# Kernel optimization log

Hardware: AMD Instinct MI355X
Metric: run time of the kernel (lower is better)

## Reference

```python
import jax, jax.numpy as jnp
import numpy as np

N_NODES = 50000
N_EDGES = 200000
D = 128
LN_EPS = 1e-5


def _layer_norm(x, g, b):
    mu = jnp.mean(x, axis=-1, keepdims=True)
    var = jnp.mean(jnp.square(x - mu), axis=-1, keepdims=True)
    return (x - mu) * jax.lax.rsqrt(var + LN_EPS) * g + b


def _mlp(x, W1, b1, W2, b2, W3, b3, g, beta):
    # 2 hidden ReLU layers + linear output + LayerNorm (MeshGraphNets style)
    h = jax.nn.relu(x @ W1 + b1)
    h = jax.nn.relu(h @ W2 + b2)
    h = h @ W3 + b3
    return _layer_norm(h, g, beta)


def setup_inputs() -> dict:
    key = jax.random.key(0)
    ks = jax.random.split(key, 12)
    d = {}
    d["node_features"] = jax.random.normal(ks[0], (N_NODES, D), dtype=jnp.float32)
    d["edge_features"] = jax.random.normal(ks[1], (N_EDGES, D), dtype=jnp.float32)
    d["senders"] = jax.random.randint(ks[2], (N_EDGES,), 0, N_NODES, dtype=jnp.int32)
    d["receivers"] = jax.random.randint(ks[3], (N_EDGES,), 0, N_NODES, dtype=jnp.int32)
    def lin(k, fan_in, fan_out):
        return jax.random.normal(k, (fan_in, fan_out), dtype=jnp.float32) / np.sqrt(fan_in)
    # edge MLP: [3D] -> D -> D -> D
    d["We1"] = lin(ks[4], 3 * D, D); d["be1"] = jnp.zeros((D,), jnp.float32)
    d["We2"] = lin(ks[5], D, D);     d["be2"] = jnp.zeros((D,), jnp.float32)
    d["We3"] = lin(ks[6], D, D);     d["be3"] = jnp.zeros((D,), jnp.float32)
    d["ge"] = jnp.ones((D,), jnp.float32); d["bege"] = jnp.zeros((D,), jnp.float32)
    # node MLP: [2D] -> D -> D -> D
    d["Wn1"] = lin(ks[7], 2 * D, D); d["bn1"] = jnp.zeros((D,), jnp.float32)
    d["Wn2"] = lin(ks[8], D, D);     d["bn2"] = jnp.zeros((D,), jnp.float32)
    d["Wn3"] = lin(ks[9], D, D);     d["bn3"] = jnp.zeros((D,), jnp.float32)
    d["gn"] = jnp.ones((D,), jnp.float32); d["begn"] = jnp.zeros((D,), jnp.float32)
    return d


def reference(node_features, edge_features, senders, receivers,
              We1, be1, We2, be2, We3, be3, ge, bege,
              Wn1, bn1, Wn2, bn2, Wn3, bn3, gn, begn):
    num_nodes = node_features.shape[0]
    # --- edge update: gather sender/receiver feats, concat, edge MLP ---
    edge_in = jnp.concatenate(
        [node_features[senders], node_features[receivers], edge_features], axis=-1)  # [E, 3D]
    new_edge = _mlp(edge_in, We1, be1, We2, be2, We3, be3, ge, bege)  # [E, D]
    # --- node update: scatter-sum aggregate, concat, node MLP ---
    agg = jax.ops.segment_sum(new_edge, receivers, num_segments=num_nodes)  # [N, D]
    node_in = jnp.concatenate([node_features, agg], axis=-1)  # [N, 2D]
    new_node = _mlp(node_in, Wn1, bn1, Wn2, bn2, Wn3, bn3, gn, begn)
    # --- residuals ---
    new_node = new_node + node_features
    new_edge = new_edge + edge_features
    return new_node, new_edge
```

## Files before the change

### kernel.cpp

```cpp
#include <hip/hip_runtime.h>
#include <hip/hip_bf16.h>

#define NNODES 50000
#define NEDGES 200000
#define DD 128
#define LN_EPS 1e-5f
#define NTH 256

typedef __attribute__((ext_vector_type(8))) short bf16x8;
typedef __attribute__((ext_vector_type(4))) float f32x4;
typedef __attribute__((ext_vector_type(16))) float f32x16;

template<int N> struct ic { static constexpr int value = N; };

__device__ __forceinline__ unsigned short bfr(float f) {
    union { __hip_bfloat16 b; unsigned short u; } v;
    v.b = __float2bfloat16(f);
    return v.u;
}

__global__ void build_wimg(const float* __restrict__ We1, const float* __restrict__ We2,
                           const float* __restrict__ We3, const float* __restrict__ Wn1,
                           const float* __restrict__ Wn2, const float* __restrict__ Wn3,
                           char* __restrict__ img_e, char* __restrict__ img_n) {
    int tid = blockIdx.x * NTH + threadIdx.x;
    const float* W; char* dst; int q;
    if      (tid <  6144) { W = We1; dst = img_e;             q = tid;         }
    else if (tid <  8192) { W = We2; dst = img_e + 12 * 8192; q = tid - 6144;  }
    else if (tid < 10240) { W = We3; dst = img_e + 16 * 8192; q = tid - 8192;  }
    else if (tid < 14336) { W = Wn1; dst = img_n;             q = tid - 10240; }
    else if (tid < 16384) { W = Wn2; dst = img_n + 8 * 8192;  q = tid - 14336; }
    else if (tid < 18432) { W = Wn3; dst = img_n + 12 * 8192; q = tid - 16384; }
    else return;
    int c = q >> 9, rem = q & 511;
    int nt = rem >> 7, r2 = rem & 127, ks = r2 >> 5, n32 = r2 & 31;
    int n = nt * 32 + n32;
    int k0 = c * 32 + ks * 8;
    unsigned short o[8];
    #pragma unroll
    for (int e = 0; e < 8; ++e)
        o[e] = bfr(W[(size_t)(k0 + e) * DD + n]);
    uint4 val;
    val.x = (unsigned)o[0] | ((unsigned)o[1] << 16);
    val.y = (unsigned)o[2] | ((unsigned)o[3] << 16);
    val.z = (unsigned)o[4] | ((unsigned)o[5] << 16);
    val.w = (unsigned)o[6] | ((unsigned)o[7] << 16);
    *(uint4*)(dst + (size_t)c * 8192 + nt * 2048 + ks * 512 + n32 * 16) = val;
}

__global__ void csr_histo(const int* __restrict__ recv, int* __restrict__ cnt) {
    int e = blockIdx.x * NTH + threadIdx.x;
    if (e < NEDGES) atomicAdd(&cnt[recv[e]], 1);
}

__global__ __launch_bounds__(1024)
void csr_scan(const int* __restrict__ cnt, int* __restrict__ off, int* __restrict__ cursor) {
    __shared__ int part[1024];
    const int t = threadIdx.x;
    const int CH = (NNODES + 1023) / 1024;
    const int base = t * CH;
    int s = 0;
    for (int i = 0; i < CH; ++i) {
        int idx = base + i;
        if (idx < NNODES) s += cnt[idx];
    }
    part[t] = s;
    __syncthreads();
    for (int d = 1; d < 1024; d <<= 1) {
        int v = (t >= d) ? part[t - d] : 0;
        __syncthreads();
        part[t] += v;
        __syncthreads();
    }
    int run = (t == 0) ? 0 : part[t - 1];
    for (int i = 0; i < CH; ++i) {
        int idx = base + i;
        if (idx < NNODES) {
            off[idx] = run; cursor[idx] = run;
            run += cnt[idx];
        }
    }
    if (t == 1023) off[NNODES] = NEDGES;
}

__global__ void csr_fill(const int* __restrict__ recv, int* __restrict__ cursor,
                         int* __restrict__ elist) {
    int e = blockIdx.x * NTH + threadIdx.x;
    if (e < NEDGES) {
        int p = atomicAdd(&cursor[recv[e]], 1);
        elist[p] = e;
    }
}

__global__ __launch_bounds__(NTH)
void aggregate(const unsigned* __restrict__ ybuf,
               const int* __restrict__ off, const int* __restrict__ elist,
               unsigned* __restrict__ aggb) {
    const int n = blockIdx.x * 4 + (threadIdx.x >> 6);
    const int l = threadIdx.x & 63;
    if (n >= NNODES) return;
    const int j0 = off[n], j1 = off[n + 1];
    float ax = 0.f, ay = 0.f, bx = 0.f, by = 0.f;
    int j = j0;
    for (; j + 1 < j1; j += 2) {
        unsigned v0 = ybuf[(size_t)elist[j] * 64 + l];
        unsigned v1 = ybuf[(size_t)elist[j + 1] * 64 + l];
        ax += __uint_as_float(v0 << 16);
        ay += __uint_as_float(v0 & 0xffff0000u);
        bx += __uint_as_float(v1 << 16);
        by += __uint_as_float(v1 & 0xffff0000u);
    }
    if (j < j1) {
        unsigned v = ybuf[(size_t)elist[j] * 64 + l];
        ax += __uint_as_float(v << 16);
        ay += __uint_as_float(v & 0xffff0000u);
    }
    float sx = ax + bx, sy = ay + by;
    aggb[(size_t)n * 64 + l] = (unsigned)bfr(sx) | ((unsigned)bfr(sy) << 16);
}

template<int MODE>
__global__ __launch_bounds__(NTH, 3)
void mgn_mfma(const float* __restrict__ nodef, const float* __restrict__ edgef,
              const int* __restrict__ senders, const int* __restrict__ receivers,
              const char* __restrict__ img,
              const float* __restrict__ b1, const float* __restrict__ b2,
              const float* __restrict__ b3,
              const float* __restrict__ gamma, const float* __restrict__ beta,
              const unsigned* __restrict__ aggb, unsigned* __restrict__ ybuf,
              float* __restrict__ outp)
{
    __shared__ char Hb[4 * 8192];

    const int t  = threadIdx.x;
    const int w  = t >> 6;
    const int l  = t & 63;
    const int ln = l & 31;
    const int hi = l >> 5;
    const int row0 = blockIdx.x * 128;
    const int gm = row0 + w * 32 + ln;
    constexpr int NROWS = (MODE == 0) ? NEDGES : NNODES;
    constexpr int NK1   = (MODE == 0) ? 12 : 8;
    constexpr int NCH   = NK1 + 8;
    const int gmc = gm < NROWS ? gm : NROWS - 1;
    const int sxH = ln & 15;

    int srow = 0, rrow = 0;
    if (MODE == 0) { srow = senders[gmc]; rrow = receivers[gmc]; }

    const f32x16 fz = {0.f,0.f,0.f,0.f,0.f,0.f,0.f,0.f,
                       0.f,0.f,0.f,0.f,0.f,0.f,0.f,0.f};
    f32x16 acc[4];
    #pragma unroll
    for (int nt = 0; nt < 4; ++nt) acc[nt] = fz;

    bf16x8 aslot[2][4];
    f32x4  bslot[2][4];

    auto loadA = [&](int h, bf16x8* dst) {
        const char* p = img + (size_t)(h >> 1) * 8192
                      + (size_t)(((h & 1) * 2 + hi) * 512) + ln * 16;
        #pragma unroll
        for (int nt = 0; nt < 4; ++nt)
            dst[nt] = *(const bf16x8*)(p + nt * 2048);
    };

    auto loadB = [&](auto CC, f32x4* dst) {
        constexpr int c = decltype(CC)::value;
        if constexpr (MODE == 1 && c >= 4) {
            const char* p = (const char*)aggb + (size_t)gmc * 256 + (c & 3) * 64 + hi * 16;
            dst[0] = *(const f32x4*)p;
            dst[2] = *(const f32x4*)(p + 32);
        } else {
            const float* base;
            if constexpr (MODE == 0) {
                base = (c < 4) ? nodef + (size_t)srow * DD
                     : (c < 8) ? nodef + (size_t)rrow * DD
                               : edgef + (size_t)gmc * DD;
            } else {
                base = nodef + (size_t)gmc * DD;
            }
            const float* p = base + (c & 3) * 32 + hi * 8;
            dst[0] = *(const f32x4*)p;
            dst[1] = *(const f32x4*)(p + 4);
            dst[2] = *(const f32x4*)(p + 16);
            dst[3] = *(const f32x4*)(p + 20);
        }
    };

    auto cvtB = [&](const f32x4* br) {
        bf16x8 r;
        #pragma unroll
        for (int i = 0; i < 4; ++i) r[i]     = (short)bfr(br[0][i]);
        #pragma unroll
        for (int i = 0; i < 4; ++i) r[4 + i] = (short)bfr(br[1][i]);
        return r;
    };

    auto loadBH = [&](int ks, int kh) {
        const char* p = Hb + w * 8192 + ln * 256
                      + (((ks * 4 + kh * 2 + hi) ^ sxH) << 4);
        return *(const bf16x8*)p;
    };

    auto getB = [&](auto CC, int kh) -> bf16x8 {
        constexpr int c = decltype(CC)::value;
        if constexpr (c >= NK1) {
            return loadBH((c - NK1) & 3, kh);
        } else if constexpr (MODE == 1 && c >= 4) {
            union { f32x4 f; bf16x8 h; } u;
            u.f = bslot[c & 1][kh * 2];
            return u.h;
        } else {
            return cvtB(&bslot[c & 1][kh * 2]);
        }
    };

    auto epiH = [&](const float* bias) {
        #pragma unroll
        for (int nt = 0; nt < 4; ++nt) {
            #pragma unroll
            for (int rq = 0; rq < 4; ++rq) {
                f32x4 bv = *(const f32x4*)(bias + nt * 32 + rq * 8 + hi * 4);
                unsigned short h[4];
                #pragma unroll
                for (int j = 0; j < 4; ++j)
                    h[j] = bfr(fmaxf(acc[nt][rq * 4 + j] + bv[j], 0.f));
                char* p = Hb + w * 8192 + ln * 256
                        + (((nt * 4 + rq) ^ sxH) << 4) + hi * 8;
                unsigned lo = (unsigned)h[0] | ((unsigned)h[1] << 16);
                unsigned hx = (unsigned)h[2] | ((unsigned)h[3] << 16);
                *(unsigned long long*)p =
                    (unsigned long long)lo | ((unsigned long long)hx << 32);
            }
            acc[nt] = fz;
        }
    };

    auto chunkfn = [&](auto CC) {
        constexpr int c = decltype(CC)::value;
        constexpr int h0 = 2 * c, h1 = 2 * c + 1;
        loadA(h1, aslot[h1 & 1]);
        {
            bf16x8 b0 = getB(CC, 0);
            #pragma unroll
            for (int nt = 0; nt < 4; ++nt)
                acc[nt] = __builtin_amdgcn_mfma_f32_32x32x16_bf16(
                    aslot[h0 & 1][nt], b0, acc[nt], 0, 0, 0);
        }
        if constexpr (h1 + 1 < 2 * NCH) loadA(h1 + 1, aslot[(h1 + 1) & 1]);
        {
            bf16x8 b1 = getB(CC, 1);
            #pragma unroll
            for (int nt = 0; nt < 4; ++nt)
                acc[nt] = __builtin_amdgcn_mfma_f32_32x32x16_bf16(
                    aslot[h1 & 1][nt], b1, acc[nt], 0, 0, 0);
        }
        if constexpr (c + 2 < NK1) loadB(ic<c + 2>{}, bslot[c & 1]);
    };

    loadB(ic<0>{}, bslot[0]);
    loadB(ic<1>{}, bslot[1]);
    loadA(0, aslot[0]);

#define CH(C)                                                                \
    if constexpr ((C) < NCH) {                                               \
        chunkfn(ic<(C)>{});                                                  \
        if constexpr ((C) == NK1 - 1) epiH(b1);                              \
        if constexpr ((C) == NK1 + 3) epiH(b2);                              \
    }
    CH(0)  CH(1)  CH(2)  CH(3)  CH(4)  CH(5)  CH(6)  CH(7)
    CH(8)  CH(9)  CH(10) CH(11) CH(12) CH(13) CH(14) CH(15)
    CH(16) CH(17) CH(18) CH(19)
#undef CH

    float vsum = 0.f, vsq = 0.f;
    #pragma unroll
    for (int nt = 0; nt < 4; ++nt) {
        #pragma unroll
        for (int rq = 0; rq < 4; ++rq) {
            f32x4 bv = *(const f32x4*)(b3 + nt * 32 + rq * 8 + hi * 4);
            #pragma unroll
            for (int j = 0; j < 4; ++j) {
                float v = acc[nt][rq * 4 + j] + bv[j];
                acc[nt][rq * 4 + j] = v;
                vsum += v; vsq += v * v;
            }
        }
    }
    vsum += __shfl_xor(vsum, 32);
    vsq  += __shfl_xor(vsq, 32);
    const float mu = vsum * (1.f / DD);
    const float rs = rsqrtf(vsq * (1.f / DD) - mu * mu + LN_EPS);

    if (gm < NROWS) {
        const float* resid = ((MODE == 0) ? edgef : nodef) + (size_t)gm * DD;
        #pragma unroll
        for (int nt = 0; nt < 4; ++nt) {
            #pragma unroll
            for (int rq = 0; rq < 4; ++rq) {
                const int n0 = nt * 32 + rq * 8 + hi * 4;
                f32x4 gv = *(const f32x4*)(gamma + n0);
                f32x4 bv = *(const f32x4*)(beta + n0);
                f32x4 rv = *(const f32x4*)(resid + n0);
                float y[4];
                f32x4 o;
                #pragma unroll
                for (int j = 0; j < 4; ++j) {
                    y[j] = (acc[nt][rq * 4 + j] - mu) * rs * gv[j] + bv[j];
                    o[j] = y[j] + rv[j];
                }
                *(f32x4*)(outp + (size_t)gm * DD + n0) = o;
                if (MODE == 0) {
                    unsigned lo = (unsigned)bfr(y[0]) | ((unsigned)bfr(y[1]) << 16);
                    unsigned hx = (unsigned)bfr(y[2]) | ((unsigned)bfr(y[3]) << 16);
                    *(unsigned long long*)((char*)ybuf + (size_t)gm * 256 + n0 * 2) =
                        (unsigned long long)lo | ((unsigned long long)hx << 32);
                }
            }
        }
    }
}

extern "C" void kernel_launch(void* const* d_in, const int* in_sizes, int n_in,
                              void* d_out, int out_size, void* d_ws, size_t ws_size,
                              hipStream_t stream) {
    const float* nodef = (const float*)d_in[0];
    const float* edgef = (const float*)d_in[1];
    const int* senders   = (const int*)d_in[2];
    const int* receivers = (const int*)d_in[3];
    const float* We1 = (const float*)d_in[4],  *be1 = (const float*)d_in[5];
    const float* We2 = (const float*)d_in[6],  *be2 = (const float*)d_in[7];
    const float* We3 = (const float*)d_in[8],  *be3 = (const float*)d_in[9];
    const float* ge  = (const float*)d_in[10], *bege = (const float*)d_in[11];
    const float* Wn1 = (const float*)d_in[12], *bn1 = (const float*)d_in[13];
    const float* Wn2 = (const float*)d_in[14], *bn2 = (const float*)d_in[15];
    const float* Wn3 = (const float*)d_in[16], *bn3 = (const float*)d_in[17];
    const float* gn  = (const float*)d_in[18], *begn = (const float*)d_in[19];

    float* out_node = (float*)d_out;
    float* out_edge = (float*)d_out + (size_t)NNODES * DD;

    char* ws = (char*)d_ws;
    size_t o = 0;
    unsigned* aggb = (unsigned*)(ws + o); o += (size_t)NNODES * 256;
    unsigned* ybuf = (unsigned*)(ws + o); o += (size_t)NEDGES * 256;
    char* img_e = ws + o;           o += 20 * 8192;
    char* img_n = ws + o;           o += 16 * 8192;
    int* cnt    = (int*)(ws + o);   o += NNODES * 4;
    int* cursor = (int*)(ws + o);   o += NNODES * 4;
    int* off    = (int*)(ws + o);   o += (NNODES + 4) * 4;
    int* elist  = (int*)(ws + o);   o += NEDGES * 4;

    hipMemsetAsync(cnt, 0, NNODES * 4, stream);
    build_wimg<<<72, NTH, 0, stream>>>(We1, We2, We3, Wn1, Wn2, Wn3, img_e, img_n);

    const int egrid = (NEDGES + NTH - 1) / NTH;
    csr_histo<<<egrid, NTH, 0, stream>>>(receivers, cnt);
    csr_scan<<<1, 1024, 0, stream>>>(cnt, off, cursor);
    csr_fill<<<egrid, NTH, 0, stream>>>(receivers, cursor, elist);

    mgn_mfma<0><<<dim3((NEDGES + 127) / 128), dim3(NTH), 0, stream>>>(
        nodef, edgef, senders, receivers, img_e,
        be1, be2, be3, ge, bege, aggb, ybuf, out_edge);

    aggregate<<<(NNODES + 3) / 4, NTH, 0, stream>>>(ybuf, off, elist, aggb);

    mgn_mfma<1><<<dim3((NNODES + 127) / 128), dim3(NTH), 0, stream>>>(
        nodef, edgef, senders, receivers, img_n,
        bn1, bn2, bn3, gn, begn, aggb, ybuf, out_node);
}
```

Before: 356.9 us.

## Pre-convert node features to bf16, deepen operand prefetch, and parallelize CSR scan

Node features are converted to bf16 once in a kernel that also builds the receiver histogram. The fused MLP kernel then gathers half-width sender/receiver rows and converts only edge features on the fly. The MLP kernel also gets triple-buffered weight loads and a six-deep B-operand prefetch, at the cost of lowering the occupancy hint from 3 to 2. Other changes: the single-block CSR scan is split into a two-level scan, bf16 rounding uses inline bit arithmetic instead of the library call, and the aggregate loop is unrolled by four. The extra conversion pass costs some bandwidth, and the larger register buffers may reduce occupancy.

```diff
diff --git a/kernel.cpp b/kernel.cpp
--- a/kernel.cpp
+++ b/kernel.cpp
@@ -1,5 +1,4 @@
 #include <hip/hip_runtime.h>
-#include <hip/hip_bf16.h>
 
 #define NNODES 50000
 #define NEDGES 200000
@@ -14,9 +13,8 @@
 template<int N> struct ic { static constexpr int value = N; };
 
 __device__ __forceinline__ unsigned short bfr(float f) {
-    union { __hip_bfloat16 b; unsigned short u; } v;
-    v.b = __float2bfloat16(f);
-    return v.u;
+    union { float f; unsigned u; } v; v.f = f;
+    return (unsigned short)((v.u + 0x7fffu + ((v.u >> 16) & 1u)) >> 16);
 }
 
 __global__ void build_wimg(const float* __restrict__ We1, const float* __restrict__ We2,
@@ -48,39 +46,63 @@
     *(uint4*)(dst + (size_t)c * 8192 + nt * 2048 + ks * 512 + n32 * 16) = val;
 }
 
-__global__ void csr_histo(const int* __restrict__ recv, int* __restrict__ cnt) {
-    int e = blockIdx.x * NTH + threadIdx.x;
-    if (e < NEDGES) atomicAdd(&cnt[recv[e]], 1);
-}
-
-__global__ __launch_bounds__(1024)
-void csr_scan(const int* __restrict__ cnt, int* __restrict__ off, int* __restrict__ cursor) {
-    __shared__ int part[1024];
-    const int t = threadIdx.x;
-    const int CH = (NNODES + 1023) / 1024;
-    const int base = t * CH;
+__global__ __launch_bounds__(NTH)
+void cvt_histo(const float* __restrict__ nodef, const int* __restrict__ recv,
+               uint4* __restrict__ nodb, int* __restrict__ cnt) {
+    const int tid0 = blockIdx.x * NTH + threadIdx.x;
+    if (tid0 < NEDGES) atomicAdd(&cnt[recv[tid0]], 1);
+    const int NG = NNODES * 16;
+    for (int g = tid0; g < NG; g += gridDim.x * NTH) {
+        f32x4 a = ((const f32x4*)nodef)[g * 2];
+        f32x4 b = ((const f32x4*)nodef)[g * 2 + 1];
+        uint4 o;
+        o.x = (unsigned)bfr(a[0]) | ((unsigned)bfr(a[1]) << 16);
+        o.y = (unsigned)bfr(a[2]) | ((unsigned)bfr(a[3]) << 16);
+        o.z = (unsigned)bfr(b[0]) | ((unsigned)bfr(b[1]) << 16);
+        o.w = (unsigned)bfr(b[2]) | ((unsigned)bfr(b[3]) << 16);
+        nodb[g] = o;
+    }
+}
+
+__global__ __launch_bounds__(NTH)
+void csr_scan1(const int* __restrict__ cnt, int* __restrict__ part) {
+    __shared__ int red[NTH];
+    const int b = blockIdx.x, t = threadIdx.x;
+    const int base = b * 196;
     int s = 0;
-    for (int i = 0; i < CH; ++i) {
+    for (int i = t; i < 196; i += NTH) {
         int idx = base + i;
         if (idx < NNODES) s += cnt[idx];
     }
-    part[t] = s;
+    red[t] = s;
     __syncthreads();
-    for (int d = 1; d < 1024; d <<= 1) {
-        int v = (t >= d) ? part[t - d] : 0;
+    for (int d = NTH / 2; d > 0; d >>= 1) {
+        if (t < d) red[t] += red[t + d];
         __syncthreads();
-        part[t] += v;
+    }
+    if (t == 0) part[b] = red[0];
+}
+
+__global__ __launch_bounds__(NTH)
+void csr_scan2(const int* __restrict__ cnt, const int* __restrict__ part,
+               int* __restrict__ off, int* __restrict__ cursor) {
+    __shared__ int sp[NTH];
+    const int t = threadIdx.x;
+    sp[t] = part[t];
+    __syncthreads();
+    for (int d = 1; d < NTH; d <<= 1) {
+        int v = (t >= d) ? sp[t - d] : 0;
         __syncthreads();
-    }
-    int run = (t == 0) ? 0 : part[t - 1];
-    for (int i = 0; i < CH; ++i) {
+        sp[t] += v;
+        __syncthreads();
+    }
+    int run = (t == 0) ? 0 : sp[t - 1];
+    const int base = t * 196;
+    for (int i = 0; i < 196; ++i) {
         int idx = base + i;
-        if (idx < NNODES) {
-            off[idx] = run; cursor[idx] = run;
-            run += cnt[idx];
-        }
-    }
-    if (t == 1023) off[NNODES] = NEDGES;
+        if (idx < NNODES) { off[idx] = run; cursor[idx] = run; run += cnt[idx]; }
+    }
+    if (t == NTH - 1) off[NNODES] = NEDGES;
 }
 
 __global__ void csr_fill(const int* __restrict__ recv, int* __restrict__ cursor,
@@ -100,34 +122,37 @@
     const int l = threadIdx.x & 63;
     if (n >= NNODES) return;
     const int j0 = off[n], j1 = off[n + 1];
-    float ax = 0.f, ay = 0.f, bx = 0.f, by = 0.f;
+    float sx = 0.f, sy = 0.f;
     int j = j0;
-    for (; j + 1 < j1; j += 2) {
-        unsigned v0 = ybuf[(size_t)elist[j] * 64 + l];
-        unsigned v1 = ybuf[(size_t)elist[j + 1] * 64 + l];
-        ax += __uint_as_float(v0 << 16);
-        ay += __uint_as_float(v0 & 0xffff0000u);
-        bx += __uint_as_float(v1 << 16);
-        by += __uint_as_float(v1 & 0xffff0000u);
-    }
-    if (j < j1) {
+    for (; j + 4 <= j1; j += 4) {
+        const int e0 = elist[j], e1 = elist[j + 1], e2 = elist[j + 2], e3 = elist[j + 3];
+        unsigned v0 = ybuf[(size_t)e0 * 64 + l];
+        unsigned v1 = ybuf[(size_t)e1 * 64 + l];
+        unsigned v2 = ybuf[(size_t)e2 * 64 + l];
+        unsigned v3 = ybuf[(size_t)e3 * 64 + l];
+        sx += __uint_as_float(v0 << 16) + __uint_as_float(v1 << 16)
+            + __uint_as_float(v2 << 16) + __uint_as_float(v3 << 16);
+        sy += __uint_as_float(v0 & 0xffff0000u) + __uint_as_float(v1 & 0xffff0000u)
+            + __uint_as_float(v2 & 0xffff0000u) + __uint_as_float(v3 & 0xffff0000u);
+    }
+    for (; j < j1; ++j) {
         unsigned v = ybuf[(size_t)elist[j] * 64 + l];
-        ax += __uint_as_float(v << 16);
-        ay += __uint_as_float(v & 0xffff0000u);
-    }
-    float sx = ax + bx, sy = ay + by;
+        sx += __uint_as_float(v << 16);
+        sy += __uint_as_float(v & 0xffff0000u);
+    }
     aggb[(size_t)n * 64 + l] = (unsigned)bfr(sx) | ((unsigned)bfr(sy) << 16);
 }
 
 template<int MODE>
-__global__ __launch_bounds__(NTH, 3)
+__global__ __launch_bounds__(NTH, 2)
 void mgn_mfma(const float* __restrict__ nodef, const float* __restrict__ edgef,
+              const unsigned short* __restrict__ nodb,
               const int* __restrict__ senders, const int* __restrict__ receivers,
               const char* __restrict__ img,
               const float* __restrict__ b1, const float* __restrict__ b2,
               const float* __restrict__ b3,
               const float* __restrict__ gamma, const float* __restrict__ beta,
-              const unsigned* __restrict__ aggb, unsigned* __restrict__ ybuf,
+              const unsigned short* __restrict__ aggb, unsigned* __restrict__ ybuf,
               float* __restrict__ outp)
 {
     __shared__ char Hb[4 * 8192];
@@ -154,8 +179,9 @@
     #pragma unroll
     for (int nt = 0; nt < 4; ++nt) acc[nt] = fz;
 
-    bf16x8 aslot[2][4];
-    f32x4  bslot[2][4];
+    bf16x8 aS[3][4];
+    bf16x8 bS[6][2];
+    f32x4  fS[2][4];
 
     auto loadA = [&](int h, bf16x8* dst) {
         const char* p = img + (size_t)(h >> 1) * 8192
@@ -165,27 +191,26 @@
             dst[nt] = *(const bf16x8*)(p + nt * 2048);
     };
 
-    auto loadB = [&](auto CC, f32x4* dst) {
+    auto loadBB = [&](auto CC, bf16x8* dst) {
         constexpr int c = decltype(CC)::value;
-        if constexpr (MODE == 1 && c >= 4) {
-            const char* p = (const char*)aggb + (size_t)gmc * 256 + (c & 3) * 64 + hi * 16;
-            dst[0] = *(const f32x4*)p;
-            dst[2] = *(const f32x4*)(p + 32);
+        const unsigned short* base;
+        if constexpr (MODE == 0) {
+            base = (c < 4) ? nodb + (size_t)srow * DD : nodb + (size_t)rrow * DD;
         } else {
-            const float* base;
-            if constexpr (MODE == 0) {
-                base = (c < 4) ? nodef + (size_t)srow * DD
-                     : (c < 8) ? nodef + (size_t)rrow * DD
-                               : edgef + (size_t)gmc * DD;
-            } else {
-                base = nodef + (size_t)gmc * DD;
-            }
-            const float* p = base + (c & 3) * 32 + hi * 8;
-            dst[0] = *(const f32x4*)p;
-            dst[1] = *(const f32x4*)(p + 4);
-            dst[2] = *(const f32x4*)(p + 16);
-            dst[3] = *(const f32x4*)(p + 20);
-        }
+            base = (c < 4) ? nodb + (size_t)gmc * DD : aggb + (size_t)gmc * DD;
+        }
+        const char* p = (const char*)base + (c & 3) * 64 + hi * 16;
+        dst[0] = *(const bf16x8*)p;
+        dst[1] = *(const bf16x8*)(p + 32);
+    };
+
+    auto loadBF = [&](auto CC, f32x4* dst) {
+        constexpr int c = decltype(CC)::value;
+        const float* p = edgef + (size_t)gmc * DD + (c & 3) * 32 + hi * 8;
+        dst[0] = *(const f32x4*)p;
+        dst[1] = *(const f32x4*)(p + 4);
+        dst[2] = *(const f32x4*)(p + 16);
+        dst[3] = *(const f32x4*)(p + 20);
     };
 
     auto cvtB = [&](const f32x4* br) {
@@ -207,12 +232,10 @@
         constexpr int c = decltype(CC)::value;
         if constexpr (c >= NK1) {
             return loadBH((c - NK1) & 3, kh);
-        } else if constexpr (MODE == 1 && c >= 4) {
-            union { f32x4 f; bf16x8 h; } u;
-            u.f = bslot[c & 1][kh * 2];
-            return u.h;
+        } else if constexpr (MODE == 0 && c >= 8) {
+            return cvtB(&fS[c & 1][kh * 2]);
         } else {
-            return cvtB(&bslot[c & 1][kh * 2]);
+            return bS[c % 6][kh];
         }
     };
 
@@ -240,28 +263,29 @@
     auto chunkfn = [&](auto CC) {
         constexpr int c = decltype(CC)::value;
         constexpr int h0 = 2 * c, h1 = 2 * c + 1;
-        loadA(h1, aslot[h1 & 1]);
+        if constexpr (h0 + 2 < 2 * NCH) loadA(h0 + 2, aS[(h0 + 2) % 3]);
         {
             bf16x8 b0 = getB(CC, 0);
             #pragma unroll
             for (int nt = 0; nt < 4; ++nt)
                 acc[nt] = __builtin_amdgcn_mfma_f32_32x32x16_bf16(
-                    aslot[h0 & 1][nt], b0, acc[nt], 0, 0, 0);
-        }
-        if constexpr (h1 + 1 < 2 * NCH) loadA(h1 + 1, aslot[(h1 + 1) & 1]);
+                    aS[h0 % 3][nt], b0, acc[nt], 0, 0, 0);
+        }
+        if constexpr (h1 + 2 < 2 * NCH) loadA(h1 + 2, aS[(h1 + 2) % 3]);
         {
             bf16x8 b1 = getB(CC, 1);
             #pragma unroll
             for (int nt = 0; nt < 4; ++nt)
                 acc[nt] = __builtin_amdgcn_mfma_f32_32x32x16_bf16(
-                    aslot[h1 & 1][nt], b1, acc[nt], 0, 0, 0);
-        }
-        if constexpr (c + 2 < NK1) loadB(ic<c + 2>{}, bslot[c & 1]);
-    };
-
-    loadB(ic<0>{}, bslot[0]);
-    loadB(ic<1>{}, bslot[1]);
-    loadA(0, aslot[0]);
+                    aS[h1 % 3][nt], b1, acc[nt], 0, 0, 0);
+        }
+        if constexpr (c + 6 < 8) loadBB(ic<c + 6>{}, bS[(c + 6) % 6]);
+        if constexpr (MODE == 0 && c >= 6 && c <= 9) loadBF(ic<c + 2>{}, fS[(c + 2) & 1]);
+    };
+
+    loadBB(ic<0>{}, bS[0]); loadBB(ic<1>{}, bS[1]); loadBB(ic<2>{}, bS[2]);
+    loadBB(ic<3>{}, bS[3]); loadBB(ic<4>{}, bS[4]); loadBB(ic<5>{}, bS[5]);
+    loadA(0, aS[0]); loadA(1, aS[1]);
 
 #define CH(C)                                                                \
     if constexpr ((C) < NCH) {                                               \
@@ -343,30 +367,31 @@
 
     char* ws = (char*)d_ws;
     size_t o = 0;
-    unsigned* aggb = (unsigned*)(ws + o); o += (size_t)NNODES * 256;
-    unsigned* ybuf = (unsigned*)(ws + o); o += (size_t)NEDGES * 256;
+    unsigned short* aggb = (unsigned short*)(ws + o); o += (size_t)NNODES * 256;
+    unsigned* ybuf = (unsigned*)(ws + o);             o += (size_t)NEDGES * 256;
+    unsigned short* nodb = (unsigned short*)(ws + o); o += (size_t)NNODES * 256;
     char* img_e = ws + o;           o += 20 * 8192;
     char* img_n = ws + o;           o += 16 * 8192;
     int* cnt    = (int*)(ws + o);   o += NNODES * 4;
     int* cursor = (int*)(ws + o);   o += NNODES * 4;
     int* off    = (int*)(ws + o);   o += (NNODES + 4) * 4;
+    int* part   = (int*)(ws + o);   o += NTH * 4;
     int* elist  = (int*)(ws + o);   o += NEDGES * 4;
 
     hipMemsetAsync(cnt, 0, NNODES * 4, stream);
+    cvt_histo<<<1024, NTH, 0, stream>>>(nodef, receivers, (uint4*)nodb, cnt);
     build_wimg<<<72, NTH, 0, stream>>>(We1, We2, We3, Wn1, Wn2, Wn3, img_e, img_n);
-
-    const int egrid = (NEDGES + NTH - 1) / NTH;
-    csr_histo<<<egrid, NTH, 0, stream>>>(receivers, cnt);
-    csr_scan<<<1, 1024, 0, stream>>>(cnt, off, cursor);
-    csr_fill<<<egrid, NTH, 0, stream>>>(receivers, cursor, elist);
+    csr_scan1<<<NTH, NTH, 0, stream>>>(cnt, part);
+    csr_scan2<<<1, NTH, 0, stream>>>(cnt, part, off, cursor);
+    csr_fill<<<(NEDGES + NTH - 1) / NTH, NTH, 0, stream>>>(receivers, cursor, elist);
 
     mgn_mfma<0><<<dim3((NEDGES + 127) / 128), dim3(NTH), 0, stream>>>(
-        nodef, edgef, senders, receivers, img_e,
+        nodef, edgef, nodb, senders, receivers, img_e,
         be1, be2, be3, ge, bege, aggb, ybuf, out_edge);
 
-    aggregate<<<(NNODES + 3) / 4, NTH, 0, stream>>>(ybuf, off, elist, aggb);
+    aggregate<<<(NNODES + 3) / 4, NTH, 0, stream>>>(ybuf, off, elist, (unsigned*)aggb);
 
     mgn_mfma<1><<<dim3((NNODES + 127) / 128), dim3(NTH), 0, stream>>>(
-        nodef, edgef, senders, receivers, img_n,
+        nodef, edgef, nodb, senders, receivers, img_n,
         bn1, bn2, bn3, gn, begn, aggb, ybuf, out_node);
 }
```

New measurement: 350.9 us. No clear change (-1.7%).
